# Kernel optimization log

Hardware: AMD Instinct MI355X
Metric: run time of the kernel (lower is better)

Reference implementation:

```python
import jax, jax.numpy as jnp
import numpy as np

B, T, E, H = 64, 512, 512, 512


def setup_inputs() -> dict:
    key = jax.random.key(0)
    ks = jax.random.split(key, 10)
    s = 1.0 / np.sqrt(H)  # torch GRU init: U(-1/sqrt(H), 1/sqrt(H))
    u = lambda k, shape: jax.random.uniform(k, shape, jnp.float32, -s, s)
    return {
        "xs": jax.random.normal(ks[0], (B, T, E), jnp.float32),
        "w_ih0": u(ks[1], (2, 3 * H, E)),
        "w_hh0": u(ks[2], (2, 3 * H, H)),
        "b_ih0": u(ks[3], (2, 3 * H)),
        "b_hh0": u(ks[4], (2, 3 * H)),
        "w_ih1": u(ks[5], (2, 3 * H, 2 * H)),
        "w_hh1": u(ks[6], (2, 3 * H, H)),
        "b_ih1": u(ks[7], (2, 3 * H)),
        "b_hh1": u(ks[8], (2, 3 * H)),
    }


def _gru_dir(x, w_ih, w_hh, b_ih, b_hh):
    # x: [B, T, D]; returns hs [B, T, H], h_T [B, H]
    h_dim = w_hh.shape[1]
    gx = jnp.einsum("btd,gd->btg", x, w_ih) + b_ih  # [B, T, 3H], all input GEMMs batched

    def step(h, gx_t):
        gh = h @ w_hh.T + b_hh
        r = jax.nn.sigmoid(gx_t[:, :h_dim] + gh[:, :h_dim])
        z = jax.nn.sigmoid(gx_t[:, h_dim:2 * h_dim] + gh[:, h_dim:2 * h_dim])
        n = jnp.tanh(gx_t[:, 2 * h_dim:] + r * gh[:, 2 * h_dim:])
        h = (1.0 - z) * n + z * h
        return h, h

    h0 = jnp.zeros((x.shape[0], h_dim), x.dtype)
    hT, hs = jax.lax.scan(step, h0, jnp.swapaxes(gx, 0, 1))
    return jnp.swapaxes(hs, 0, 1), hT


def _bidir_layer(x, w_ih, w_hh, b_ih, b_hh):
    hs_f, h_f = _gru_dir(x, w_ih[0], w_hh[0], b_ih[0], b_hh[0])
    hs_b, h_b = _gru_dir(x[:, ::-1], w_ih[1], w_hh[1], b_ih[1], b_hh[1])
    hs_b = hs_b[:, ::-1]
    return jnp.concatenate([hs_f, hs_b], axis=-1), jnp.stack([h_f, h_b])


def reference(xs, w_ih0, w_hh0, b_ih0, b_hh0, w_ih1, w_hh1, b_ih1, b_hh1):
    h0_out, hy0 = _bidir_layer(xs, w_ih0, w_hh0, b_ih0, b_hh0)
    h1_out, hy1 = _bidir_layer(h0_out, w_ih1, w_hh1, b_ih1, b_hh1)
    hy = jnp.concatenate([hy0, hy1], axis=0)  # [n_layers*2, B, H]
    # dropout p=0.0 -> identity
    return (h1_out, hy)
```

## Files before the change

kernel.cpp:

```cpp
#include <hip/hip_runtime.h>
#include <stdint.h>

#define Bq 64
#define Tq 512
#define Hq 512
#define G3 1536

typedef unsigned short u16;
typedef uint32_t u32;
typedef unsigned long long u64;
typedef __attribute__((ext_vector_type(8))) short bf16x8;
typedef __attribute__((ext_vector_type(4))) float f32x4;

__device__ __forceinline__ float bf2f(u16 v){ unsigned u = ((unsigned)v)<<16; float f; __builtin_memcpy(&f,&u,4); return f; }
__device__ __forceinline__ u16 f2bf(float f){ unsigned u; __builtin_memcpy(&u,&f,4); u += 0x7fffu + ((u>>16)&1u); return (u16)(u>>16); }

__global__ void detect_k(const u16* __restrict__ xs, int* __restrict__ flag){
  __shared__ int cnt;
  if (threadIdx.x==0) cnt = 0;
  __syncthreads();
  int good = 0;
  for (int i = threadIdx.x; i < 4096; i += 256) {
    u16 v = xs[2*i];
    int e = (v>>7)&0xFF;
    if (e==0 || (e>=100 && e<=140)) good++;
  }
  atomicAdd(&cnt, good);
  __syncthreads();
  if (threadIdx.x==0) flag[0] = (cnt > 3600) ? 1 : 0;
}

template<int K, int AMODE, int OUTF32>
__global__ __launch_bounds__(256,1) void gemm_gx(const void* __restrict__ Araw,
        const void* __restrict__ Wraw, const void* __restrict__ braw,
        void* __restrict__ outraw, const int* __restrict__ dflag)
{
  __shared__ __align__(16) u16 Ah[64*72];
  __shared__ __align__(16) u16 Al[64*72];
  __shared__ __align__(16) u16 Wh[64*72];
  __shared__ __align__(16) u16 Wl[64*72];
  const int bf16in = dflag[0];
  const bool useAlo = (AMODE==0) && !bf16in;
  const bool useWlo = !bf16in;
  const int dir = blockIdx.z;
  const int tid = threadIdx.x;
  const int m0 = blockIdx.x*64, n0 = blockIdx.y*64;
  const int wave = tid>>6, lane = tid&63;
  const int wm = (wave>>1)*32, wn = (wave&1)*32;
  f32x4 acc[2][2] = {};

  for (int kb=0; kb<K/64; kb++) {
    if (AMODE==0 && !bf16in) {
      const float* Af = (const float*)Araw;
      #pragma unroll
      for (int it=0; it<4; it++) {
        int c = it*256 + tid;
        int r = c>>4, cc = (c&15)*4;
        float4 v = *(const float4*)&Af[(size_t)(m0+r)*K + kb*64 + cc];
        u16 h0=f2bf(v.x), h1=f2bf(v.y), h2=f2bf(v.z), h3=f2bf(v.w);
        *(ushort4*)&Ah[r*72+cc] = make_ushort4(h0,h1,h2,h3);
        *(ushort4*)&Al[r*72+cc] = make_ushort4(
            f2bf(v.x-bf2f(h0)), f2bf(v.y-bf2f(h1)),
            f2bf(v.z-bf2f(h2)), f2bf(v.w-bf2f(h3)));
      }
    } else {
      const u16* Ab = (const u16*)Araw;
      #pragma unroll
      for (int it=0; it<2; it++) {
        int c = it*256 + tid;
        int r = c>>3, cc = (c&7)*8;
        *(bf16x8*)&Ah[r*72+cc] = *(const bf16x8*)&Ab[(size_t)(m0+r)*K + kb*64 + cc];
      }
    }
    if (!bf16in) {
      const float* Wf = (const float*)Wraw + (size_t)dir*G3*K;
      #pragma unroll
      for (int it=0; it<4; it++) {
        int c = it*256 + tid;
        int r = c>>4, cc = (c&15)*4;
        float4 v = *(const float4*)&Wf[(size_t)(n0+r)*K + kb*64 + cc];
        u16 h0=f2bf(v.x), h1=f2bf(v.y), h2=f2bf(v.z), h3=f2bf(v.w);
        *(ushort4*)&Wh[r*72+cc] = make_ushort4(h0,h1,h2,h3);
        *(ushort4*)&Wl[r*72+cc] = make_ushort4(
            f2bf(v.x-bf2f(h0)), f2bf(v.y-bf2f(h1)),
            f2bf(v.z-bf2f(h2)), f2bf(v.w-bf2f(h3)));
      }
    } else {
      const u16* Wb = (const u16*)Wraw + (size_t)dir*G3*K;
      #pragma unroll
      for (int it=0; it<2; it++) {
        int c = it*256 + tid;
        int r = c>>3, cc = (c&7)*8;
        *(bf16x8*)&Wh[r*72+cc] = *(const bf16x8*)&Wb[(size_t)(n0+r)*K + kb*64 + cc];
      }
    }
    __syncthreads();
    #pragma unroll
    for (int ks=0; ks<2; ks++) {
      int ko = ks*32 + (lane>>4)*8;
      bf16x8 a0 = *(const bf16x8*)&Ah[(wm    + (lane&15))*72 + ko];
      bf16x8 a1 = *(const bf16x8*)&Ah[(wm+16 + (lane&15))*72 + ko];
      bf16x8 b0 = *(const bf16x8*)&Wh[(wn    + (lane&15))*72 + ko];
      bf16x8 b1 = *(const bf16x8*)&Wh[(wn+16 + (lane&15))*72 + ko];
      acc[0][0] = __builtin_amdgcn_mfma_f32_16x16x32_bf16(a0,b0,acc[0][0],0,0,0);
      acc[0][1] = __builtin_amdgcn_mfma_f32_16x16x32_bf16(a0,b1,acc[0][1],0,0,0);
      acc[1][0] = __builtin_amdgcn_mfma_f32_16x16x32_bf16(a1,b0,acc[1][0],0,0,0);
      acc[1][1] = __builtin_amdgcn_mfma_f32_16x16x32_bf16(a1,b1,acc[1][1],0,0,0);
      if (useAlo) {
        bf16x8 c0 = *(const bf16x8*)&Al[(wm    + (lane&15))*72 + ko];
        bf16x8 c1 = *(const bf16x8*)&Al[(wm+16 + (lane&15))*72 + ko];
        acc[0][0] = __builtin_amdgcn_mfma_f32_16x16x32_bf16(c0,b0,acc[0][0],0,0,0);
        acc[0][1] = __builtin_amdgcn_mfma_f32_16x16x32_bf16(c0,b1,acc[0][1],0,0,0);
        acc[1][0] = __builtin_amdgcn_mfma_f32_16x16x32_bf16(c1,b0,acc[1][0],0,0,0);
        acc[1][1] = __builtin_amdgcn_mfma_f32_16x16x32_bf16(c1,b1,acc[1][1],0,0,0);
      }
      if (useWlo) {
        bf16x8 d0 = *(const bf16x8*)&Wl[(wn    + (lane&15))*72 + ko];
        bf16x8 d1 = *(const bf16x8*)&Wl[(wn+16 + (lane&15))*72 + ko];
        acc[0][0] = __builtin_amdgcn_mfma_f32_16x16x32_bf16(a0,d0,acc[0][0],0,0,0);
        acc[0][1] = __builtin_amdgcn_mfma_f32_16x16x32_bf16(a0,d1,acc[0][1],0,0,0);
        acc[1][0] = __builtin_amdgcn_mfma_f32_16x16x32_bf16(a1,d0,acc[1][0],0,0,0);
        acc[1][1] = __builtin_amdgcn_mfma_f32_16x16x32_bf16(a1,d1,acc[1][1],0,0,0);
      }
    }
    __syncthreads();
  }
  #pragma unroll
  for (int i=0;i<2;i++) {
    #pragma unroll
    for (int j=0;j<2;j++) {
      int nn = n0 + wn + j*16 + (lane&15);
      float bv = bf16in ? bf2f(((const u16*)braw)[dir*G3 + nn])
                        : ((const float*)braw)[dir*G3 + nn];
      #pragma unroll
      for (int r=0;r<4;r++) {
        int mm = m0 + wm + i*16 + (lane>>4)*4 + r;
        int b = mm >> 9, t = mm & 511;
        size_t oi = ((size_t)(dir*Tq + t)*Bq + b)*G3 + nn;
        float v = acc[i][j][r] + bv;
        if (OUTF32) ((float*)outraw)[oi] = v;
        else        ((u16*)outraw)[oi]   = f2bf(v);
      }
    }
  }
}

template<int LAYER, int GXF32>
__global__ __launch_bounds__(384,1) void gru_scan(const void* __restrict__ whh,
        const void* __restrict__ bhh, const void* __restrict__ gx,
        u16* __restrict__ hs0, void* __restrict__ dout,
        u32* __restrict__ hexw, int* __restrict__ flags,
        const int* __restrict__ dflag)
{
  extern __shared__ char smem[];
  u16*   wlds = (u16*)smem;
  u16*   ht   = (u16*)(smem + 99840);
  float* ghl  = (float*)(smem + 116480);
  float* bhl  = (float*)(smem + 122880);
  u32*   htw  = (u32*)ht;

  const int bf16in = dflag[0];
  const int tid = threadIdx.x;
  const int bx  = blockIdx.x;
  const int dir = bx>>6, group=(bx>>4)&3, slice=bx&15;
  const int jbase = slice*32, bg0 = group*16;
  int* fl = flags + (dir*4+group)*16;

  if (!bf16in) {
    const float* wf = (const float*)whh + (size_t)dir*G3*Hq;
    for (int c = tid; c < 96*128; c += 384) {
      int r = c>>7, q = (c&127)*4;
      int gate = r>>5, jj = r&31;
      float4 v = *(const float4*)&wf[(size_t)(gate*512 + jbase + jj)*Hq + q];
      *(ushort4*)&wlds[r*520 + q] = make_ushort4(f2bf(v.x),f2bf(v.y),f2bf(v.z),f2bf(v.w));
    }
  } else {
    const u16* wb = (const u16*)whh + (size_t)dir*G3*Hq;
    for (int c = tid; c < 96*64; c += 384) {
      int r = c>>6, cc = (c&63)*8;
      int gate = r>>5, jj = r&31;
      *(bf16x8*)&wlds[r*520 + cc] = *(const bf16x8*)&wb[(size_t)(gate*512 + jbase + jj)*Hq + cc];
    }
  }
  if (tid < 96) {
    int gate = tid>>5, jj = tid&31;
    int off = dir*G3 + gate*512 + jbase + jj;
    bhl[tid] = bf16in ? bf2f(((const u16*)bhh)[off]) : ((const float*)bhh)[off];
  }
  __syncthreads();

  const int lane = tid&63;
  const int n0w = (tid>>6)*16;

  const int e0 = tid,       b0 = e0>>5, j0 = e0&31;
  const int e1 = tid + 384, b1 = e1>>5, j1 = e1&31;
  const bool has1 = (tid < 128);
  float h0 = 0.f, h1v = 0.f;
  float gr0,gz0,gn0, gr1,gz1,gn1;
  gr0=gz0=gn0=gr1=gz1=gn1=0.f;

  auto ldgx = [&](int t_in_, int b, int j, float& gr, float& gz, float& gn){
    size_t gbase = ((size_t)(dir*Tq + t_in_)*Bq + (bg0 + b))*G3 + jbase + j;
    if (GXF32) { const float* gp=(const float*)gx + gbase; gr=gp[0]; gz=gp[512]; gn=gp[1024]; }
    else       { const u16* gp=(const u16*)gx + gbase; gr=bf2f(gp[0]); gz=bf2f(gp[512]); gn=bf2f(gp[1024]); }
  };
  {
    int t0 = dir ? (Tq-1) : 0;
    ldgx(t0, b0, j0, gr0, gz0, gn0);
    if (has1) ldgx(t0, b1, j1, gr1, gz1, gn1);
  }

  for (int s=0; s<Tq; s++) {
    const int t_in = dir ? (Tq-1-s) : s;
    if (tid < 16) {
      while (__hip_atomic_fetch_add(&fl[tid], 0, __ATOMIC_RELAXED, __HIP_MEMORY_SCOPE_AGENT) < 6*s) {
        __builtin_amdgcn_s_sleep(1);
      }
    }
    __syncthreads();
    {
      const u32 rb = (u32)(((s&1)*2 + dir)*Bq + bg0)*256u;
      for (int c = tid; c < 16*128; c += 384) {
        int r = c>>7, w2 = c&127;
        u64 v = __hip_atomic_fetch_add((u64*)&hexw[rb + (u32)r*256u + (u32)(2*w2)],
                                  (u64)0, __ATOMIC_RELAXED, __HIP_MEMORY_SCOPE_AGENT);
        *(u64*)&htw[r*260 + 2*w2] = v;
      }
    }
    __syncthreads();
    f32x4 acc = {0.f,0.f,0.f,0.f};
    #pragma unroll
    for (int kk=0; kk<16; kk++) {
      int ko = kk*32 + (lane>>4)*8;
      bf16x8 a = *(const bf16x8*)&ht  [ (lane&15)       *520 + ko];
      bf16x8 b = *(const bf16x8*)&wlds[(n0w + (lane&15))*520 + ko];
      acc = __builtin_amdgcn_mfma_f32_16x16x32_bf16(a,b,acc,0,0,0);
    }
    #pragma unroll
    for (int r=0;r<4;r++) ghl[((lane>>4)*4 + r)*100 + n0w + (lane&15)] = acc[r];
    __syncthreads();

    const u32 rb2 = (u32)((((s+1)&1)*2 + dir)*Bq + bg0)*256u;
    float hn0 = 0.f, hn1 = 0.f;
    u16 hb0 = 0, hb1 = 0;
    {
      float rr = gr0 + ghl[b0*100 + j0]      + bhl[j0];
      float zz = gz0 + ghl[b0*100 + 32 + j0] + bhl[32 + j0];
      float gh =       ghl[b0*100 + 64 + j0] + bhl[64 + j0];
      float r = 1.f/(1.f + __expf(-rr));
      float z = 1.f/(1.f + __expf(-zz));
      float x = gn0 + r*gh;
      x = fminf(fmaxf(x, -15.f), 15.f);
      float e2 = __expf(2.f*x);
      float n = (e2 - 1.f)/(e2 + 1.f);
      hn0 = (1.f - z)*n + z*h0;
      h0 = hn0; hb0 = f2bf(hn0);
    }
    if (has1) {
      float rr = gr1 + ghl[b1*100 + j1]      + bhl[j1];
      float zz = gz1 + ghl[b1*100 + 32 + j1] + bhl[32 + j1];
      float gh =       ghl[b1*100 + 64 + j1] + bhl[64 + j1];
      float r = 1.f/(1.f + __expf(-rr));
      float z = 1.f/(1.f + __expf(-zz));
      float x = gn1 + r*gh;
      x = fminf(fmaxf(x, -15.f), 15.f);
      float e2 = __expf(2.f*x);
      float n = (e2 - 1.f)/(e2 + 1.f);
      hn1 = (1.f - z)*n + z*h1v;
      h1v = hn1; hb1 = f2bf(hn1);
    }
    {
      int v0 = hb0;
      int up0 = __shfl_down(v0, 1);
      if ((tid & 1) == 0) {
        (void)__hip_atomic_exchange(&hexw[rb2 + (u32)b0*256u + (u32)(slice*16 + (j0>>1))],
                           (u32)(v0 & 0xffff) | ((u32)up0 << 16),
                           __ATOMIC_RELAXED, __HIP_MEMORY_SCOPE_AGENT);
      }
      if (has1) {
        int v1 = hb1;
        int up1 = __shfl_down(v1, 1);
        if ((tid & 1) == 0) {
          (void)__hip_atomic_exchange(&hexw[rb2 + (u32)b1*256u + (u32)(slice*16 + (j1>>1))],
                             (u32)(v1 & 0xffff) | ((u32)up1 << 16),
                             __ATOMIC_RELAXED, __HIP_MEMORY_SCOPE_AGENT);
        }
      }
    }
    asm volatile("s_waitcnt vmcnt(0)" ::: "memory");
    if ((tid & 63) == 0) {
      (void)__hip_atomic_fetch_add(&fl[slice], 1, __ATOMIC_RELAXED, __HIP_MEMORY_SCOPE_AGENT);
    }

    if (s+1 < Tq) {
      int tn = dir ? (Tq-2-s) : (s+1);
      ldgx(tn, b0, j0, gr0, gz0, gn0);
      if (has1) ldgx(tn, b1, j1, gr1, gz1, gn1);
    }

    {
      int bg = bg0 + b0;
      size_t oi = ((size_t)bg*Tq + t_in)*1024 + dir*512 + jbase + j0;
      if (LAYER==0) {
        __builtin_nontemporal_store(hb0, &hs0[oi]);
      } else {
        if (bf16in) __builtin_nontemporal_store(hb0, &((u16*)dout)[oi]);
        else        __builtin_nontemporal_store(hn0, &((float*)dout)[oi]);
      }
      if (s == Tq-1) {
        size_t hyi = (size_t)Bq*Tq*1024 + ((size_t)(LAYER*2 + dir)*Bq + bg)*512 + jbase + j0;
        if (bf16in) ((u16*)dout)[hyi] = hb0;
        else        ((float*)dout)[hyi] = hn0;
      }
    }
    if (has1) {
      int bg = bg0 + b1;
      size_t oi = ((size_t)bg*Tq + t_in)*1024 + dir*512 + jbase + j1;
      if (LAYER==0) {
        __builtin_nontemporal_store(hb1, &hs0[oi]);
      } else {
        if (bf16in) __builtin_nontemporal_store(hb1, &((u16*)dout)[oi]);
        else        __builtin_nontemporal_store(hn1, &((float*)dout)[oi]);
      }
      if (s == Tq-1) {
        size_t hyi = (size_t)Bq*Tq*1024 + ((size_t)(LAYER*2 + dir)*Bq + bg)*512 + jbase + j1;
        if (bf16in) ((u16*)dout)[hyi] = hb1;
        else        ((float*)dout)[hyi] = hn1;
      }
    }
  }
}

__global__ void init_k(u32* hexw, int* flags){
  int i = blockIdx.x*256 + threadIdx.x;
  if (i < 2*2*Bq*256) hexw[i] = 0;
  if (i < 128) flags[i] = 0;
}

extern "C" void kernel_launch(void* const* d_in, const int* in_sizes, int n_in,
                              void* d_out, int out_size, void* d_ws, size_t ws_size,
                              hipStream_t stream)
{
  const void* xs    = d_in[0];
  const void* w_ih0 = d_in[1];
  const void* w_hh0 = d_in[2];
  const void* b_ih0 = d_in[3];
  const void* b_hh0 = d_in[4];
  const void* w_ih1 = d_in[5];
  const void* w_hh1 = d_in[6];
  const void* b_ih1 = d_in[7];
  const void* b_hh1 = d_in[8];
  (void)in_sizes; (void)n_in; (void)out_size;

  char* ws   = (char*)d_ws;
  int* dflag = (int*)ws;
  int* flags = (int*)(ws + 256);
  u32* hexw  = (u32*)(ws + 1024);
  void* gx   = (void*)(ws + 263168ULL);
  const bool gxf32 = ws_size >= 263168ULL + 402653184ULL;
  u16* hs0   = (u16*)d_out;

  hipFuncSetAttribute((const void*)gru_scan<0,0>, hipFuncAttributeMaxDynamicSharedMemorySize, 123264);
  hipFuncSetAttribute((const void*)gru_scan<1,0>, hipFuncAttributeMaxDynamicSharedMemorySize, 123264);
  hipFuncSetAttribute((const void*)gru_scan<0,1>, hipFuncAttributeMaxDynamicSharedMemorySize, 123264);
  hipFuncSetAttribute((const void*)gru_scan<1,1>, hipFuncAttributeMaxDynamicSharedMemorySize, 123264);

  dim3 gg(Tq*Bq/64, G3/64, 2);

  detect_k<<<1, 256, 0, stream>>>((const u16*)xs, dflag);
  init_k<<<512, 256, 0, stream>>>(hexw, flags);
  if (gxf32) {
    gemm_gx<512,0,1><<<gg, 256, 0, stream>>>(xs, w_ih0, b_ih0, gx, dflag);
    gru_scan<0,1><<<128, 384, 123264, stream>>>(w_hh0, b_hh0, gx, hs0, d_out, hexw, flags, dflag);
    gemm_gx<1024,1,1><<<gg, 256, 0, stream>>>(hs0, w_ih1, b_ih1, gx, dflag);
    init_k<<<512, 256, 0, stream>>>(hexw, flags);
    gru_scan<1,1><<<128, 384, 123264, stream>>>(w_hh1, b_hh1, gx, hs0, d_out, hexw, flags, dflag);
  } else {
    gemm_gx<512,0,0><<<gg, 256, 0, stream>>>(xs, w_ih0, b_ih0, gx, dflag);
    gru_scan<0,0><<<128, 384, 123264, stream>>>(w_hh0, b_hh0, gx, hs0, d_out, hexw, flags, dflag);
    gemm_gx<1024,1,0><<<gg, 256, 0, stream>>>(hs0, w_ih1, b_ih1, gx, dflag);
    init_k<<<512, 256, 0, stream>>>(hexw, flags);
    gru_scan<1,0><<<128, 384, 123264, stream>>>(w_hh1, b_hh1, gx, hs0, d_out, hexw, flags, dflag);
  }
}
```

Before: 6.973 ms.

## Keep recurrent weight slice in registers and pack hidden-state exchange into 64-bit atomics

Each wave now loads its 16-row slice of W_hh into 16 bf16x8 registers once, instead of staging all 96 rows in LDS and rereading them every timestep. This removes the per-step LDS traffic for the B operand of the MFMA and shrinks dynamic shared memory to about 23 KB. Separately, the hidden-state publish step gathers four bf16 values with shuffles and writes them with one 64-bit atomic exchange, halving the number of cross-block atomics. The cost is higher VGPR pressure (64 extra registers per lane) and extra shuffles.

```diff
diff --git a/kernel.cpp b/kernel.cpp
--- a/kernel.cpp
+++ b/kernel.cpp
@@ -153,10 +153,9 @@
         const int* __restrict__ dflag)
 {
   extern __shared__ char smem[];
-  u16*   wlds = (u16*)smem;
-  u16*   ht   = (u16*)(smem + 99840);
-  float* ghl  = (float*)(smem + 116480);
-  float* bhl  = (float*)(smem + 122880);
+  u16*   ht   = (u16*)smem;
+  float* ghl  = (float*)(smem + 16640);
+  float* bhl  = (float*)(smem + 23040);
   u32*   htw  = (u32*)ht;
 
   const int bf16in = dflag[0];
@@ -166,20 +165,34 @@
   const int jbase = slice*32, bg0 = group*16;
   int* fl = flags + (dir*4+group)*16;
 
-  if (!bf16in) {
-    const float* wf = (const float*)whh + (size_t)dir*G3*Hq;
-    for (int c = tid; c < 96*128; c += 384) {
-      int r = c>>7, q = (c&127)*4;
-      int gate = r>>5, jj = r&31;
-      float4 v = *(const float4*)&wf[(size_t)(gate*512 + jbase + jj)*Hq + q];
-      *(ushort4*)&wlds[r*520 + q] = make_ushort4(f2bf(v.x),f2bf(v.y),f2bf(v.z),f2bf(v.w));
-    }
-  } else {
-    const u16* wb = (const u16*)whh + (size_t)dir*G3*Hq;
-    for (int c = tid; c < 96*64; c += 384) {
-      int r = c>>6, cc = (c&63)*8;
-      int gate = r>>5, jj = r&31;
-      *(bf16x8*)&wlds[r*520 + cc] = *(const bf16x8*)&wb[(size_t)(gate*512 + jbase + jj)*Hq + cc];
+  const int lane = tid&63;
+  const int n0w = (tid>>6)*16;
+
+  bf16x8 wreg[16];
+  {
+    const int n = n0w + (lane&15);
+    const int gate = n>>5, jj = n&31;
+    const int khalf = (lane>>4)*8;
+    if (!bf16in) {
+      const float* wf = (const float*)whh + (size_t)dir*G3*Hq
+                      + (size_t)(gate*512 + jbase + jj)*Hq;
+      #pragma unroll
+      for (int kk=0; kk<16; kk++) {
+        float4 v0 = *(const float4*)&wf[kk*32 + khalf];
+        float4 v1 = *(const float4*)&wf[kk*32 + khalf + 4];
+        bf16x8 w;
+        w[0]=(short)f2bf(v0.x); w[1]=(short)f2bf(v0.y);
+        w[2]=(short)f2bf(v0.z); w[3]=(short)f2bf(v0.w);
+        w[4]=(short)f2bf(v1.x); w[5]=(short)f2bf(v1.y);
+        w[6]=(short)f2bf(v1.z); w[7]=(short)f2bf(v1.w);
+        wreg[kk] = w;
+      }
+    } else {
+      const u16* wb = (const u16*)whh + (size_t)dir*G3*Hq
+                    + (size_t)(gate*512 + jbase + jj)*Hq;
+      #pragma unroll
+      for (int kk=0; kk<16; kk++)
+        wreg[kk] = *(const bf16x8*)&wb[kk*32 + khalf];
     }
   }
   if (tid < 96) {
@@ -188,9 +201,6 @@
     bhl[tid] = bf16in ? bf2f(((const u16*)bhh)[off]) : ((const float*)bhh)[off];
   }
   __syncthreads();
-
-  const int lane = tid&63;
-  const int n0w = (tid>>6)*16;
 
   const int e0 = tid,       b0 = e0>>5, j0 = e0&31;
   const int e1 = tid + 384, b1 = e1>>5, j1 = e1&31;
@@ -232,9 +242,8 @@
     #pragma unroll
     for (int kk=0; kk<16; kk++) {
       int ko = kk*32 + (lane>>4)*8;
-      bf16x8 a = *(const bf16x8*)&ht  [ (lane&15)       *520 + ko];
-      bf16x8 b = *(const bf16x8*)&wlds[(n0w + (lane&15))*520 + ko];
-      acc = __builtin_amdgcn_mfma_f32_16x16x32_bf16(a,b,acc,0,0,0);
+      bf16x8 a = *(const bf16x8*)&ht[(lane&15)*520 + ko];
+      acc = __builtin_amdgcn_mfma_f32_16x16x32_bf16(a,wreg[kk],acc,0,0,0);
     }
     #pragma unroll
     for (int r=0;r<4;r++) ghl[((lane>>4)*4 + r)*100 + n0w + (lane&15)] = acc[r];
@@ -270,20 +279,24 @@
       h1v = hn1; hb1 = f2bf(hn1);
     }
     {
-      int v0 = hb0;
-      int up0 = __shfl_down(v0, 1);
-      if ((tid & 1) == 0) {
-        (void)__hip_atomic_exchange(&hexw[rb2 + (u32)b0*256u + (u32)(slice*16 + (j0>>1))],
-                           (u32)(v0 & 0xffff) | ((u32)up0 << 16),
-                           __ATOMIC_RELAXED, __HIP_MEMORY_SCOPE_AGENT);
+      u32 p1 = (u32)__shfl_down((int)hb0, 1);
+      u32 p2 = (u32)__shfl_down((int)hb0, 2);
+      u32 p3 = (u32)__shfl_down((int)hb0, 3);
+      if ((tid & 3) == 0) {
+        u64 pk = (u64)hb0 | ((u64)(p1 & 0xffffu) << 16)
+               | ((u64)(p2 & 0xffffu) << 32) | ((u64)(p3 & 0xffffu) << 48);
+        (void)__hip_atomic_exchange((u64*)&hexw[rb2 + (u32)b0*256u + (u32)(slice*16 + (j0>>1))],
+                                    pk, __ATOMIC_RELAXED, __HIP_MEMORY_SCOPE_AGENT);
       }
       if (has1) {
-        int v1 = hb1;
-        int up1 = __shfl_down(v1, 1);
-        if ((tid & 1) == 0) {
-          (void)__hip_atomic_exchange(&hexw[rb2 + (u32)b1*256u + (u32)(slice*16 + (j1>>1))],
-                             (u32)(v1 & 0xffff) | ((u32)up1 << 16),
-                             __ATOMIC_RELAXED, __HIP_MEMORY_SCOPE_AGENT);
+        u32 q1 = (u32)__shfl_down((int)hb1, 1);
+        u32 q2 = (u32)__shfl_down((int)hb1, 2);
+        u32 q3 = (u32)__shfl_down((int)hb1, 3);
+        if ((tid & 3) == 0) {
+          u64 pk = (u64)hb1 | ((u64)(q1 & 0xffffu) << 16)
+                 | ((u64)(q2 & 0xffffu) << 32) | ((u64)(q3 & 0xffffu) << 48);
+          (void)__hip_atomic_exchange((u64*)&hexw[rb2 + (u32)b1*256u + (u32)(slice*16 + (j1>>1))],
+                                      pk, __ATOMIC_RELAXED, __HIP_MEMORY_SCOPE_AGENT);
         }
       }
     }
@@ -360,26 +373,21 @@
   const bool gxf32 = ws_size >= 263168ULL + 402653184ULL;
   u16* hs0   = (u16*)d_out;
 
-  hipFuncSetAttribute((const void*)gru_scan<0,0>, hipFuncAttributeMaxDynamicSharedMemorySize, 123264);
-  hipFuncSetAttribute((const void*)gru_scan<1,0>, hipFuncAttributeMaxDynamicSharedMemorySize, 123264);
-  hipFuncSetAttribute((const void*)gru_scan<0,1>, hipFuncAttributeMaxDynamicSharedMemorySize, 123264);
-  hipFuncSetAttribute((const void*)gru_scan<1,1>, hipFuncAttributeMaxDynamicSharedMemorySize, 123264);
-
   dim3 gg(Tq*Bq/64, G3/64, 2);
 
   detect_k<<<1, 256, 0, stream>>>((const u16*)xs, dflag);
   init_k<<<512, 256, 0, stream>>>(hexw, flags);
   if (gxf32) {
     gemm_gx<512,0,1><<<gg, 256, 0, stream>>>(xs, w_ih0, b_ih0, gx, dflag);
-    gru_scan<0,1><<<128, 384, 123264, stream>>>(w_hh0, b_hh0, gx, hs0, d_out, hexw, flags, dflag);
+    gru_scan<0,1><<<128, 384, 23424, stream>>>(w_hh0, b_hh0, gx, hs0, d_out, hexw, flags, dflag);
     gemm_gx<1024,1,1><<<gg, 256, 0, stream>>>(hs0, w_ih1, b_ih1, gx, dflag);
     init_k<<<512, 256, 0, stream>>>(hexw, flags);
-    gru_scan<1,1><<<128, 384, 123264, stream>>>(w_hh1, b_hh1, gx, hs0, d_out, hexw, flags, dflag);
+    gru_scan<1,1><<<128, 384, 23424, stream>>>(w_hh1, b_hh1, gx, hs0, d_out, hexw, flags, dflag);
   } else {
     gemm_gx<512,0,0><<<gg, 256, 0, stream>>>(xs, w_ih0, b_ih0, gx, dflag);
-    gru_scan<0,0><<<128, 384, 123264, stream>>>(w_hh0, b_hh0, gx, hs0, d_out, hexw, flags, dflag);
+    gru_scan<0,0><<<128, 384, 23424, stream>>>(w_hh0, b_hh0, gx, hs0, d_out, hexw, flags, dflag);
     gemm_gx<1024,1,0><<<gg, 256, 0, stream>>>(hs0, w_ih1, b_ih1, gx, dflag);
     init_k<<<512, 256, 0, stream>>>(hexw, flags);
-    gru_scan<1,0><<<128, 384, 123264, stream>>>(w_hh1, b_hh1, gx, hs0, d_out, hexw, flags, dflag);
-  }
-}
+    gru_scan<1,0><<<128, 384, 23424, stream>>>(w_hh1, b_hh1, gx, hs0, d_out, hexw, flags, dflag);
+  }
+}
```

Result: faster. 6.819 ms (-2.2%).
